# Kernel tuning notes

Hardware: AMD Instinct MI355X
Metric: run time of the kernel (lower is better)

The kernel has to match this reference:

```python
import jax, jax.numpy as jnp
import numpy as np

B, T, C = 4, 2048, 2048
H, KV, D = 16, 4, 128          # head_dim = C // H
G = H // KV                     # query heads per kv head
ROPE_BASE = 10000.0


def _rope_tables(T, D, dtype):
    inv_freq = 1.0 / (ROPE_BASE ** (jnp.arange(0, D, 2, dtype=jnp.float32) / D))
    t = jnp.arange(T, dtype=jnp.float32)
    freqs = jnp.outer(t, inv_freq)                 # [T, D/2]
    emb = jnp.concatenate([freqs, freqs], axis=-1) # [T, D]
    return jnp.cos(emb).astype(dtype), jnp.sin(emb).astype(dtype)


def _rotate_half(x):
    x1, x2 = x[..., : x.shape[-1] // 2], x[..., x.shape[-1] // 2 :]
    return jnp.concatenate([-x2, x1], axis=-1)


def setup_inputs() -> dict:
    key = jax.random.key(0)
    ks = jax.random.split(key, 5)
    s = 0.02
    return {
        "x":  jax.random.normal(ks[0], (B, T, C), dtype=jnp.float32),
        "Wq": jax.random.normal(ks[1], (C, H * D), dtype=jnp.float32) * s,
        "Wk": jax.random.normal(ks[2], (C, KV * D), dtype=jnp.float32) * s,
        "Wv": jax.random.normal(ks[3], (C, KV * D), dtype=jnp.float32) * s,
        "Wo": jax.random.normal(ks[4], (C, C), dtype=jnp.float32) * s,
    }


def reference(x, Wq, Wk, Wv, Wo):
    Bc, Tc, Cc = x.shape
    q = (x @ Wq).reshape(Bc, Tc, H, D).transpose(0, 2, 1, 3)   # [B,H,T,D]
    k = (x @ Wk).reshape(Bc, Tc, KV, D).transpose(0, 2, 1, 3)  # [B,KV,T,D]
    v = (x @ Wv).reshape(Bc, Tc, KV, D).transpose(0, 2, 1, 3)  # [B,KV,T,D]

    cos, sin = _rope_tables(Tc, D, x.dtype)                    # [T,D]
    q = q * cos + _rotate_half(q) * sin
    k = k * cos + _rotate_half(k) * sin

    # GQA: broadcast KV heads instead of materializing repeat_interleave.
    # repeat_interleave over head dim == view q as [B,KV,G,T,D] sharing kv head.
    qg = q.reshape(Bc, KV, G, Tc, D)
    scale = D ** -0.5
    scores = jnp.einsum("bkgtd,bksd->bkgts", qg, k) * scale    # [B,KV,G,T,T]
    causal = jnp.tril(jnp.ones((Tc, Tc), dtype=bool))
    scores = jnp.where(causal, scores, jnp.finfo(scores.dtype).min)
    att = jax.nn.softmax(scores, axis=-1)
    out = jnp.einsum("bkgts,bksd->bkgtd", att, v)              # [B,KV,G,T,D]
    out = out.reshape(Bc, H, Tc, D).transpose(0, 2, 1, 3).reshape(Bc, Tc, Cc)
    return out @ Wo
```

## Files before the change

kernel.cpp:

```cpp
#include <hip/hip_runtime.h>
#include <cstdint>

#define DEV __device__ __forceinline__

typedef __attribute__((ext_vector_type(4))) float f32x4;
typedef __attribute__((ext_vector_type(4))) float float4v;
typedef __attribute__((ext_vector_type(8))) short bf16x8;
typedef __attribute__((ext_vector_type(4))) unsigned short ushort4v;
typedef __attribute__((ext_vector_type(2))) unsigned int uint2v;
typedef unsigned short u16;

static constexpr int Bb = 4, Tt = 2048, Hh = 16, KVh = 4, Dd = 128;
static constexpr int NQKV = 3072;

DEV u16 f2bf(float x) {
    union { float f; unsigned u; } v; v.f = x;
    unsigned r = v.u + 0x7FFF + ((v.u >> 16) & 1);
    return (u16)(r >> 16);
}
DEV float bf2f(u16 b) {
    union { unsigned u; float f; } v; v.u = ((unsigned)b) << 16;
    return v.f;
}
DEV unsigned cvtpk(float lo, float hi) {
    unsigned d;
    asm("v_cvt_pk_bf16_f32 %0, %1, %2" : "=v"(d) : "v"(lo), "v"(hi));
    return d;
}

typedef const void __attribute__((address_space(1)))* gas1;
typedef void __attribute__((address_space(3)))* las3;
DEV void gload16(const void* g, void* l) {
    __builtin_amdgcn_global_load_lds((gas1)g, (las3)l, 16, 0, 0);
}

__global__ __launch_bounds__(256) void cast_k(const float* __restrict__ x, u16* __restrict__ xb, long n4) {
    long id = (long)blockIdx.x * 256 + threadIdx.x;
    if (id >= n4) return;
    float4v v = *(const float4v*)&x[id * 4];
    ushort4v o;
    o[0] = f2bf(v[0]); o[1] = f2bf(v[1]); o[2] = f2bf(v[2]); o[3] = f2bf(v[3]);
    *(ushort4v*)&xb[id * 4] = o;
}

__global__ __launch_bounds__(256) void twt_k(const float* __restrict__ W, u16* __restrict__ Wt, int K, int N) {
    __shared__ float tile[32][33];
    int tx = threadIdx.x, ty = threadIdx.y;
    long n0 = (long)blockIdx.x * 32, k0 = (long)blockIdx.y * 32;
#pragma unroll
    for (int j = 0; j < 4; j++)
        tile[ty + j * 8][tx] = W[(k0 + ty + j * 8) * (long)N + n0 + tx];
    __syncthreads();
#pragma unroll
    for (int j = 0; j < 4; j++)
        Wt[(n0 + ty + j * 8) * (long)K + k0 + tx] = f2bf(tile[tx][ty + j * 8]);
}

__global__ __launch_bounds__(256) void tv_k(const u16* __restrict__ qkv, u16* __restrict__ vt) {
    __shared__ u16 tile[32][33];
    int tx = threadIdx.x, ty = threadIdx.y;
    int d0 = blockIdx.x * 32;
    int t0 = blockIdx.y * 32;
    int bk = blockIdx.z;
    int b = bk >> 2, kv = bk & 3;
#pragma unroll
    for (int j = 0; j < 4; j++)
        tile[ty + j * 8][tx] = qkv[(long)(b * Tt + t0 + ty + j * 8) * NQKV + 2560 + kv * Dd + d0 + tx];
    __syncthreads();
#pragma unroll
    for (int j = 0; j < 4; j++)
        vt[((long)(b * KVh + kv) * Dd + d0 + ty + j * 8) * Tt + t0 + tx] = tile[tx][ty + j * 8];
}

__global__ __launch_bounds__(256) void tables_k(float* __restrict__ cosb, float* __restrict__ sinb) {
    int id = blockIdx.x * 256 + threadIdx.x;
    int t = id >> 6, i = id & 63;
    float inv = powf(10000.0f, -(float)i * (1.0f / 64.0f));
    float f = (float)t * inv;
    cosb[id] = cosf(f);
    sinb[id] = sinf(f);
}

__global__ __launch_bounds__(256) void rope_k(u16* __restrict__ p, const float* __restrict__ cosb,
                                              const float* __restrict__ sinb, int nh, float scale, int total8,
                                              long rowstride, int colbase) {
    int id = blockIdx.x * 256 + threadIdx.x;
    if (id >= total8) return;
    int i8 = id & 7;
    int bth = id >> 3;
    int row = bth / nh;
    int t = row % Tt;
    u16* ptr = p + (long)row * rowstride + colbase + (bth % nh) * Dd + i8 * 8;
    ushort4v a0 = *(ushort4v*)&ptr[0];
    ushort4v a1 = *(ushort4v*)&ptr[4];
    ushort4v b0 = *(ushort4v*)&ptr[64];
    ushort4v b1 = *(ushort4v*)&ptr[68];
    const float4v c0 = *(const float4v*)&cosb[t * 64 + i8 * 8];
    const float4v c1 = *(const float4v*)&cosb[t * 64 + i8 * 8 + 4];
    const float4v s0 = *(const float4v*)&sinb[t * 64 + i8 * 8];
    const float4v s1 = *(const float4v*)&sinb[t * 64 + i8 * 8 + 4];
    ushort4v oa0, oa1, ob0, ob1;
#pragma unroll
    for (int j = 0; j < 4; j++) {
        float x1 = bf2f(a0[j]), x2 = bf2f(b0[j]);
        oa0[j] = f2bf((x1 * c0[j] - x2 * s0[j]) * scale);
        ob0[j] = f2bf((x2 * c0[j] + x1 * s0[j]) * scale);
        float y1 = bf2f(a1[j]), y2 = bf2f(b1[j]);
        oa1[j] = f2bf((y1 * c1[j] - y2 * s1[j]) * scale);
        ob1[j] = f2bf((y2 * c1[j] + y1 * s1[j]) * scale);
    }
    *(ushort4v*)&ptr[0] = oa0;
    *(ushort4v*)&ptr[4] = oa1;
    *(ushort4v*)&ptr[64] = ob0;
    *(ushort4v*)&ptr[68] = ob1;
}

template <int F32OUT>
__global__ __launch_bounds__(512) void gemm_k(const u16* __restrict__ A, const u16* __restrict__ Bt,
                                              void* __restrict__ Cout, int M, int N, int K) {
    __shared__ u16 lds[3][24576];
    const int tid = threadIdx.x;
    const int lane = tid & 63;
    const int w = __builtin_amdgcn_readfirstlane(tid >> 6);
    const int wm = w >> 1, wn = w & 1;
    const long m0 = (long)blockIdx.x * 256;
    const long n0 = (long)blockIdx.y * 128;
    const int NT = K >> 6;
    const int l8 = lane >> 3, s8 = lane & 7;
    const int fr = lane & 15, kg = lane >> 4;

    auto stageA = [&](int t) {
        u16* base = lds[t % 3];
        const long ko = (long)t * 64;
#pragma unroll
        for (int c4 = 0; c4 < 4; c4++) {
            int c = w * 4 + c4;
            int row = c * 8 + l8;
            int slog = s8 ^ (l8 & 7);
            gload16(A + (m0 + row) * (long)K + ko + slog * 8, base + c * 512);
        }
    };
    auto stageB = [&](int t) {
        u16* base = lds[t % 3];
        const long ko = (long)t * 64;
#pragma unroll
        for (int c2 = 0; c2 < 2; c2++) {
            int c = w * 2 + c2;
            int row = c * 8 + l8;
            int slog = s8 ^ (l8 & 7);
            gload16(Bt + (n0 + row) * (long)K + ko + slog * 8, base + 16384 + c * 512);
        }
    };

    f32x4 acc[4][4] = {};
    stageA(0); stageB(0);
    if (NT > 1) {
        stageA(1); stageB(1);
        asm volatile("s_waitcnt vmcnt(6)" ::: "memory");
    } else {
        asm volatile("s_waitcnt vmcnt(0)" ::: "memory");
    }
    __builtin_amdgcn_s_barrier();

    for (int t = 0; t < NT; ++t) {
        const u16* sa = lds[t % 3];
        const u16* sb = sa + 16384;
        {
            bf16x8 af[4], bfr[4];
#pragma unroll
            for (int i = 0; i < 4; i++) {
                const int row = wm * 64 + i * 16 + fr;
                af[i] = *(const bf16x8*)&sa[row * 64 + ((kg ^ (row & 7)) * 8)];
                const int col = wn * 64 + i * 16 + fr;
                bfr[i] = *(const bf16x8*)&sb[col * 64 + ((kg ^ (col & 7)) * 8)];
            }
            if (t + 2 < NT) stageA(t + 2);
            __builtin_amdgcn_s_barrier();
            __builtin_amdgcn_s_setprio(1);
#pragma unroll
            for (int i = 0; i < 4; i++)
#pragma unroll
                for (int j = 0; j < 4; j++)
                    acc[i][j] = __builtin_amdgcn_mfma_f32_16x16x32_bf16(af[i], bfr[j], acc[i][j], 0, 0, 0);
            __builtin_amdgcn_s_setprio(0);
            __builtin_amdgcn_s_barrier();
        }
        {
            bf16x8 af[4], bfr[4];
#pragma unroll
            for (int i = 0; i < 4; i++) {
                const int row = wm * 64 + i * 16 + fr;
                af[i] = *(const bf16x8*)&sa[row * 64 + (((4 + kg) ^ (row & 7)) * 8)];
                const int col = wn * 64 + i * 16 + fr;
                bfr[i] = *(const bf16x8*)&sb[col * 64 + (((4 + kg) ^ (col & 7)) * 8)];
            }
            if (t + 2 < NT) stageB(t + 2);
            if (t + 2 < NT)
                asm volatile("s_waitcnt vmcnt(6)" ::: "memory");
            else if (t + 1 < NT)
                asm volatile("s_waitcnt vmcnt(0)" ::: "memory");
            __builtin_amdgcn_s_barrier();
            __builtin_amdgcn_s_setprio(1);
#pragma unroll
            for (int i = 0; i < 4; i++)
#pragma unroll
                for (int j = 0; j < 4; j++)
                    acc[i][j] = __builtin_amdgcn_mfma_f32_16x16x32_bf16(af[i], bfr[j], acc[i][j], 0, 0, 0);
            __builtin_amdgcn_s_setprio(0);
            __builtin_amdgcn_s_barrier();
        }
    }

    const int orow = (lane >> 4) * 4, ocol = lane & 15;
#pragma unroll
    for (int i = 0; i < 4; i++)
#pragma unroll
        for (int j = 0; j < 4; j++) {
            long r = m0 + wm * 64 + i * 16 + orow;
            long c = n0 + wn * 64 + j * 16 + ocol;
#pragma unroll
            for (int t = 0; t < 4; t++) {
                if (F32OUT)
                    ((float*)Cout)[(r + t) * N + c] = acc[i][j][t];
                else
                    ((u16*)Cout)[(r + t) * N + c] = f2bf(acc[i][j][t]);
            }
        }
}

__global__ __launch_bounds__(256, 3) void attn_k(const u16* __restrict__ qkv,
                                                 const u16* __restrict__ vt, u16* __restrict__ o) {
    __shared__ u16 kl[2][4096];
    __shared__ u16 vl[2][4096];
    __shared__ u16 pT[4][2][16][36];
    const int tid = threadIdx.x;
    const int lane = tid & 63;
    const int w = tid >> 6;
    const int kvb = blockIdx.x;
    const int kv = kvb & 3, b = kvb >> 2;
    const int qt = 63 - (int)blockIdx.y;
    const int q0 = qt * 32;
    const int h = kv * 4 + w;
    const int fr = lane & 15, kg = lane >> 4;
    const long HD = (long)Hh * Dd;
    const long QS = (long)NQKV;
    const long kbase = (long)b * Tt * QS + 2048 + (long)kv * Dd;
    const long vbase = ((long)(b * KVh + kv)) * (long)Dd * Tt;
    const long qbase = (long)(b * Tt + q0) * QS + (long)h * Dd;
    const long obase = (long)(b * Tt + q0) * HD + (long)h * Dd;

    auto stage = [&](int bb, int it) {
        const int s0 = it * 32;
        const int lh = lane >> 4;
#pragma unroll
        for (int j = 0; j < 2; j++) {
            int c = j * 4 + w;
            int row = c * 4 + lh;
            int c16 = (lane & 15) ^ (row & 7);
            gload16(qkv + kbase + (long)(s0 + row) * QS + c16 * 8, &kl[bb][c * 512]);
        }
#pragma unroll
        for (int j = 0; j < 2; j++) {
            int c = j * 4 + w;
            int rowp = c * 4 + lh;
            int c16u = (lane & 15) ^ (rowp & 7);
            int r = rowp * 4 + (c16u >> 2);
            gload16(vt + vbase + (long)r * Tt + s0 + (c16u & 3) * 8, &vl[bb][c * 512]);
        }
    };

    bf16x8 qa[2][4];
#pragma unroll
    for (int qi = 0; qi < 2; qi++)
#pragma unroll
        for (int kc = 0; kc < 4; kc++)
            qa[qi][kc] = *(const bf16x8*)&qkv[qbase + (long)(qi * 16 + fr) * QS + kc * 32 + kg * 8];

    f32x4 ot[8][2] = {};
    float mr0 = -1e30f, mr1 = -1e30f, lr0 = 0.0f, lr1 = 0.0f;
    const int nt = qt + 1;

    stage(0, 0);
    __syncthreads();
    int cur = 0;
    for (int it = 0; it < nt; ++it) {
        if (it + 1 < nt) stage(cur ^ 1, it + 1);
        const int s0 = it * 32;
        f32x4 st[2][2] = {};
        __builtin_amdgcn_s_setprio(1);
#pragma unroll
        for (int kf = 0; kf < 2; kf++) {
            const int rr = kf * 16 + fr;
            bf16x8 ka[4];
#pragma unroll
            for (int kc = 0; kc < 4; kc++)
                ka[kc] = *(const bf16x8*)&kl[cur][rr * 128 + (((kc * 4 + kg) ^ (rr & 7)) * 8)];
#pragma unroll
            for (int kc = 0; kc < 4; kc++) {
                st[kf][0] = __builtin_amdgcn_mfma_f32_16x16x32_bf16(ka[kc], qa[0][kc], st[kf][0], 0, 0, 0);
                st[kf][1] = __builtin_amdgcn_mfma_f32_16x16x32_bf16(ka[kc], qa[1][kc], st[kf][1], 0, 0, 0);
            }
        }
        __builtin_amdgcn_s_setprio(0);
        if (it == nt - 1) {
#pragma unroll
            for (int kf = 0; kf < 2; kf++)
#pragma unroll
                for (int qi = 0; qi < 2; qi++) {
                    const int qq = q0 + qi * 16 + fr;
                    const int kb0 = s0 + kf * 16 + kg * 4;
#pragma unroll
                    for (int r = 0; r < 4; r++)
                        if (kb0 + r > qq) st[kf][qi][r] = -1e30f;
                }
        }
        float tm0 = st[0][0][0], tm1 = st[0][1][0];
#pragma unroll
        for (int kf = 0; kf < 2; kf++)
#pragma unroll
            for (int r = 0; r < 4; r++)
                if (kf | r) {
                    tm0 = fmaxf(tm0, st[kf][0][r]);
                    tm1 = fmaxf(tm1, st[kf][1][r]);
                }
        tm0 = fmaxf(tm0, __shfl_xor(tm0, 16)); tm0 = fmaxf(tm0, __shfl_xor(tm0, 32));
        tm1 = fmaxf(tm1, __shfl_xor(tm1, 16)); tm1 = fmaxf(tm1, __shfl_xor(tm1, 32));
        if (__any(fmaxf(tm0 - mr0, tm1 - mr1) > 8.0f)) {
            float mn0 = fmaxf(mr0, tm0), mn1 = fmaxf(mr1, tm1);
            float al0 = __builtin_amdgcn_exp2f(mr0 - mn0);
            float al1 = __builtin_amdgcn_exp2f(mr1 - mn1);
            mr0 = mn0; mr1 = mn1;
            lr0 *= al0; lr1 *= al1;
#pragma unroll
            for (int df = 0; df < 8; df++) { ot[df][0] *= al0; ot[df][1] *= al1; }
        }
        float rs0 = 0.0f, rs1 = 0.0f;
#pragma unroll
        for (int kf = 0; kf < 2; kf++)
#pragma unroll
            for (int r = 0; r < 4; r++) {
                st[kf][0][r] = __builtin_amdgcn_exp2f(st[kf][0][r] - mr0); rs0 += st[kf][0][r];
                st[kf][1][r] = __builtin_amdgcn_exp2f(st[kf][1][r] - mr1); rs1 += st[kf][1][r];
            }
        rs0 += __shfl_xor(rs0, 16); rs0 += __shfl_xor(rs0, 32);
        rs1 += __shfl_xor(rs1, 16); rs1 += __shfl_xor(rs1, 32);
        lr0 += rs0; lr1 += rs1;
#pragma unroll
        for (int qi = 0; qi < 2; qi++) {
            uint2v w0;
            w0[0] = cvtpk(st[0][qi][0], st[0][qi][1]);
            w0[1] = cvtpk(st[0][qi][2], st[0][qi][3]);
            *(uint2v*)&pT[w][qi][fr][kg * 4] = w0;
            uint2v w1;
            w1[0] = cvtpk(st[1][qi][0], st[1][qi][1]);
            w1[1] = cvtpk(st[1][qi][2], st[1][qi][3]);
            *(uint2v*)&pT[w][qi][fr][16 + kg * 4] = w1;
        }
        {
            bf16x8 bq0 = *(const bf16x8*)&pT[w][0][fr][kg * 8];
            bf16x8 bq1 = *(const bf16x8*)&pT[w][1][fr][kg * 8];
            __builtin_amdgcn_s_setprio(1);
#pragma unroll
            for (int df = 0; df < 8; df++) {
                const int r = df * 16 + fr;
                const int rowp = r >> 2;
                const int c16 = (((r & 3) * 4 + kg) ^ (rowp & 7));
                bf16x8 va = *(const bf16x8*)&vl[cur][rowp * 128 + c16 * 8];
                ot[df][0] = __builtin_amdgcn_mfma_f32_16x16x32_bf16(va, bq0, ot[df][0], 0, 0, 0);
                ot[df][1] = __builtin_amdgcn_mfma_f32_16x16x32_bf16(va, bq1, ot[df][1], 0, 0, 0);
            }
            __builtin_amdgcn_s_setprio(0);
        }
        __syncthreads();
        cur ^= 1;
    }
    const float il0 = 1.0f / lr0, il1 = 1.0f / lr1;
#pragma unroll
    for (int df = 0; df < 8; df++) {
        uint2v w0, w1;
        w0[0] = cvtpk(ot[df][0][0] * il0, ot[df][0][1] * il0);
        w0[1] = cvtpk(ot[df][0][2] * il0, ot[df][0][3] * il0);
        w1[0] = cvtpk(ot[df][1][0] * il1, ot[df][1][1] * il1);
        w1[1] = cvtpk(ot[df][1][2] * il1, ot[df][1][3] * il1);
        *(uint2v*)&o[obase + (long)(fr) * HD + df * 16 + kg * 4] = w0;
        *(uint2v*)&o[obase + (long)(16 + fr) * HD + df * 16 + kg * 4] = w1;
    }
}

extern "C" void kernel_launch(void* const* d_in, const int* in_sizes, int n_in,
                              void* d_out, int out_size, void* d_ws, size_t ws_size,
                              hipStream_t stream) {
    (void)in_sizes; (void)n_in; (void)out_size; (void)ws_size;
    const float* x = (const float*)d_in[0];
    const float* Wq = (const float*)d_in[1];
    const float* Wk = (const float*)d_in[2];
    const float* Wv = (const float*)d_in[3];
    const float* Wo = (const float*)d_in[4];

    char* ws = (char*)d_ws;
    u16* xb   = (u16*)(ws + 0);
    u16* vtb  = (u16*)(ws + 50331648);
    u16* wqt  = (u16*)(ws + 58720256);
    u16* wkt  = (u16*)(ws + 67108864);
    u16* wvt  = (u16*)(ws + 69206016);
    u16* wot  = (u16*)(ws + 71303168);
    float* cosb = (float*)(ws + 79691776);
    float* sinb = (float*)(ws + 80216064);
    u16* qkv = (u16*)d_out;

    dim3 tb(32, 8);
    cast_k<<<16384, 256, 0, stream>>>(x, xb, 4194304);
    twt_k<<<dim3(64, 64), tb, 0, stream>>>(Wq, wqt, 2048, 2048);
    twt_k<<<dim3(16, 64), tb, 0, stream>>>(Wk, wkt, 2048, 512);
    twt_k<<<dim3(16, 64), tb, 0, stream>>>(Wv, wvt, 2048, 512);
    twt_k<<<dim3(64, 64), tb, 0, stream>>>(Wo, wot, 2048, 2048);
    tables_k<<<512, 256, 0, stream>>>(cosb, sinb);

    gemm_k<0><<<dim3(32, 24), 512, 0, stream>>>(xb, wqt, qkv, 8192, NQKV, 2048);

    rope_k<<<4096, 256, 0, stream>>>(qkv, cosb, sinb, 16, 0.1275174316f, 1048576, NQKV, 0);
    rope_k<<<1024, 256, 0, stream>>>(qkv, cosb, sinb, 4, 1.0f, 262144, NQKV, 2048);
    tv_k<<<dim3(4, 64, 16), tb, 0, stream>>>(qkv, vtb);

    attn_k<<<dim3(16, 64), 256, 0, stream>>>(qkv, vtb, xb);

    gemm_k<1><<<dim3(32, 16), 512, 0, stream>>>(xb, wot, d_out, 8192, 2048, 2048);
}
```

Baseline: 344.5 us.

## Software-pipeline QK^T of next tile with softmax and PV of current

```diff
diff --git a/kernel.cpp b/kernel.cpp
--- a/kernel.cpp
+++ b/kernel.cpp
@@ -230,7 +230,7 @@
 
 __global__ __launch_bounds__(256, 3) void attn_k(const u16* __restrict__ qkv,
                                                  const u16* __restrict__ vt, u16* __restrict__ o) {
-    __shared__ u16 kl[2][4096];
+    __shared__ u16 kl[3][4096];
     __shared__ u16 vl[2][4096];
     __shared__ u16 pT[4][2][16][36];
     const int tid = threadIdx.x;
@@ -249,23 +249,27 @@
     const long qbase = (long)(b * Tt + q0) * QS + (long)h * Dd;
     const long obase = (long)(b * Tt + q0) * HD + (long)h * Dd;
 
-    auto stage = [&](int bb, int it) {
-        const int s0 = it * 32;
+    auto stage_k = [&](int t) {
+        const int s0 = t * 32;
         const int lh = lane >> 4;
 #pragma unroll
         for (int j = 0; j < 2; j++) {
             int c = j * 4 + w;
             int row = c * 4 + lh;
             int c16 = (lane & 15) ^ (row & 7);
-            gload16(qkv + kbase + (long)(s0 + row) * QS + c16 * 8, &kl[bb][c * 512]);
-        }
+            gload16(qkv + kbase + (long)(s0 + row) * QS + c16 * 8, &kl[t % 3][c * 512]);
+        }
+    };
+    auto stage_v = [&](int t) {
+        const int s0 = t * 32;
+        const int lh = lane >> 4;
 #pragma unroll
         for (int j = 0; j < 2; j++) {
             int c = j * 4 + w;
             int rowp = c * 4 + lh;
             int c16u = (lane & 15) ^ (rowp & 7);
             int r = rowp * 4 + (c16u >> 2);
-            gload16(vt + vbase + (long)r * Tt + s0 + (c16u & 3) * 8, &vl[bb][c * 512]);
+            gload16(vt + vbase + (long)r * Tt + s0 + (c16u & 3) * 8, &vl[t & 1][c * 512]);
         }
     };
 
@@ -275,33 +279,40 @@
 #pragma unroll
         for (int kc = 0; kc < 4; kc++)
             qa[qi][kc] = *(const bf16x8*)&qkv[qbase + (long)(qi * 16 + fr) * QS + kc * 32 + kg * 8];
+
+    auto qkcomp = [&](const u16* klbuf, f32x4 (&st)[2][2]) {
+        __builtin_amdgcn_s_setprio(1);
+#pragma unroll
+        for (int kf = 0; kf < 2; kf++) {
+            const int rr = kf * 16 + fr;
+            bf16x8 ka[4];
+#pragma unroll
+            for (int kc = 0; kc < 4; kc++)
+                ka[kc] = *(const bf16x8*)&klbuf[rr * 128 + (((kc * 4 + kg) ^ (rr & 7)) * 8)];
+#pragma unroll
+            for (int kc = 0; kc < 4; kc++) {
+                st[kf][0] = __builtin_amdgcn_mfma_f32_16x16x32_bf16(ka[kc], qa[0][kc], st[kf][0], 0, 0, 0);
+                st[kf][1] = __builtin_amdgcn_mfma_f32_16x16x32_bf16(ka[kc], qa[1][kc], st[kf][1], 0, 0, 0);
+            }
+        }
+        __builtin_amdgcn_s_setprio(0);
+    };
 
     f32x4 ot[8][2] = {};
     float mr0 = -1e30f, mr1 = -1e30f, lr0 = 0.0f, lr1 = 0.0f;
     const int nt = qt + 1;
 
-    stage(0, 0);
+    stage_k(0); stage_v(0);
+    if (nt > 1) stage_k(1);
     __syncthreads();
-    int cur = 0;
+
+    f32x4 stA[2][2] = {};
+    qkcomp(kl[0], stA);
+
     for (int it = 0; it < nt; ++it) {
-        if (it + 1 < nt) stage(cur ^ 1, it + 1);
+        if (it + 2 < nt) stage_k(it + 2);
+        if (it + 1 < nt) stage_v(it + 1);
         const int s0 = it * 32;
-        f32x4 st[2][2] = {};
-        __builtin_amdgcn_s_setprio(1);
-#pragma unroll
-        for (int kf = 0; kf < 2; kf++) {
-            const int rr = kf * 16 + fr;
-            bf16x8 ka[4];
-#pragma unroll
-            for (int kc = 0; kc < 4; kc++)
-                ka[kc] = *(const bf16x8*)&kl[cur][rr * 128 + (((kc * 4 + kg) ^ (rr & 7)) * 8)];
-#pragma unroll
-            for (int kc = 0; kc < 4; kc++) {
-                st[kf][0] = __builtin_amdgcn_mfma_f32_16x16x32_bf16(ka[kc], qa[0][kc], st[kf][0], 0, 0, 0);
-                st[kf][1] = __builtin_amdgcn_mfma_f32_16x16x32_bf16(ka[kc], qa[1][kc], st[kf][1], 0, 0, 0);
-            }
-        }
-        __builtin_amdgcn_s_setprio(0);
         if (it == nt - 1) {
 #pragma unroll
             for (int kf = 0; kf < 2; kf++)
@@ -311,17 +322,17 @@
                     const int kb0 = s0 + kf * 16 + kg * 4;
 #pragma unroll
                     for (int r = 0; r < 4; r++)
-                        if (kb0 + r > qq) st[kf][qi][r] = -1e30f;
+                        if (kb0 + r > qq) stA[kf][qi][r] = -1e30f;
                 }
         }
-        float tm0 = st[0][0][0], tm1 = st[0][1][0];
+        float tm0 = stA[0][0][0], tm1 = stA[0][1][0];
 #pragma unroll
         for (int kf = 0; kf < 2; kf++)
 #pragma unroll
             for (int r = 0; r < 4; r++)
                 if (kf | r) {
-                    tm0 = fmaxf(tm0, st[kf][0][r]);
-                    tm1 = fmaxf(tm1, st[kf][1][r]);
+                    tm0 = fmaxf(tm0, stA[kf][0][r]);
+                    tm1 = fmaxf(tm1, stA[kf][1][r]);
                 }
         tm0 = fmaxf(tm0, __shfl_xor(tm0, 16)); tm0 = fmaxf(tm0, __shfl_xor(tm0, 32));
         tm1 = fmaxf(tm1, __shfl_xor(tm1, 16)); tm1 = fmaxf(tm1, __shfl_xor(tm1, 32));
@@ -339,8 +350,8 @@
         for (int kf = 0; kf < 2; kf++)
 #pragma unroll
             for (int r = 0; r < 4; r++) {
-                st[kf][0][r] = __builtin_amdgcn_exp2f(st[kf][0][r] - mr0); rs0 += st[kf][0][r];
-                st[kf][1][r] = __builtin_amdgcn_exp2f(st[kf][1][r] - mr1); rs1 += st[kf][1][r];
+                stA[kf][0][r] = __builtin_amdgcn_exp2f(stA[kf][0][r] - mr0); rs0 += stA[kf][0][r];
+                stA[kf][1][r] = __builtin_amdgcn_exp2f(stA[kf][1][r] - mr1); rs1 += stA[kf][1][r];
             }
         rs0 += __shfl_xor(rs0, 16); rs0 += __shfl_xor(rs0, 32);
         rs1 += __shfl_xor(rs1, 16); rs1 += __shfl_xor(rs1, 32);
@@ -348,14 +359,16 @@
 #pragma unroll
         for (int qi = 0; qi < 2; qi++) {
             uint2v w0;
-            w0[0] = cvtpk(st[0][qi][0], st[0][qi][1]);
-            w0[1] = cvtpk(st[0][qi][2], st[0][qi][3]);
+            w0[0] = cvtpk(stA[0][qi][0], stA[0][qi][1]);
+            w0[1] = cvtpk(stA[0][qi][2], stA[0][qi][3]);
             *(uint2v*)&pT[w][qi][fr][kg * 4] = w0;
             uint2v w1;
-            w1[0] = cvtpk(st[1][qi][0], st[1][qi][1]);
-            w1[1] = cvtpk(st[1][qi][2], st[1][qi][3]);
+            w1[0] = cvtpk(stA[1][qi][0], stA[1][qi][1]);
+            w1[1] = cvtpk(stA[1][qi][2], stA[1][qi][3]);
             *(uint2v*)&pT[w][qi][fr][16 + kg * 4] = w1;
         }
+        f32x4 stB[2][2] = {};
+        if (it + 1 < nt) qkcomp(kl[(it + 1) % 3], stB);
         {
             bf16x8 bq0 = *(const bf16x8*)&pT[w][0][fr][kg * 8];
             bf16x8 bq1 = *(const bf16x8*)&pT[w][1][fr][kg * 8];
@@ -365,14 +378,18 @@
                 const int r = df * 16 + fr;
                 const int rowp = r >> 2;
                 const int c16 = (((r & 3) * 4 + kg) ^ (rowp & 7));
-                bf16x8 va = *(const bf16x8*)&vl[cur][rowp * 128 + c16 * 8];
+                bf16x8 va = *(const bf16x8*)&vl[it & 1][rowp * 128 + c16 * 8];
                 ot[df][0] = __builtin_amdgcn_mfma_f32_16x16x32_bf16(va, bq0, ot[df][0], 0, 0, 0);
                 ot[df][1] = __builtin_amdgcn_mfma_f32_16x16x32_bf16(va, bq1, ot[df][1], 0, 0, 0);
             }
             __builtin_amdgcn_s_setprio(0);
         }
         __syncthreads();
-        cur ^= 1;
+#pragma unroll
+        for (int kf = 0; kf < 2; kf++)
+#pragma unroll
+            for (int qi = 0; qi < 2; qi++)
+                stA[kf][qi] = stB[kf][qi];
     }
     const float il0 = 1.0f / lr0, il1 = 1.0f / lr1;
 #pragma unroll
```

New measurement: 341.9 us. Within noise of the previous version (-0.7%).
